# Kernel optimization log

Measured on AMD Instinct MI355X. Metric: run time of the kernel, lower is better.

The kernel has to match this reference:

```python
import jax, jax.numpy as jnp
import numpy as np

EPS = 1e-6
C = 0.05            # curvature
TEMPERATURE = 0.1
ALPHA_D = 0.5       # current_epoch = 0 -> alpha stays at init value


def setup_inputs() -> dict:
    key = jax.random.key(0)
    k1, k2 = jax.random.split(key)
    B, D = 1024, 128
    # scale so norms stay well inside the Poincare ball (radius 1/sqrt(c) ~ 4.47)
    z_hyp = jax.random.normal(k1, (B, D), dtype=jnp.float32) * 0.05
    z_hyp_prime = jax.random.normal(k2, (B, D), dtype=jnp.float32) * 0.05
    return {"z_hyp": z_hyp, "z_hyp_prime": z_hyp_prime}


def _pairwise_hyp_distance(zx, zy, c):
    """d(x_i, y_j) = 2/sqrt(c) * atanh(sqrt(c) * ||mobius_add(-x_i, y_j)||) for all pairs."""
    x = -zx[:, None, :]          # [B, 1, D]  (neg_x in the original)
    y = zy[None, :, :]           # [1, B, D]
    x2 = jnp.sum(x * x, axis=-1, keepdims=True)   # [B, 1, 1]
    y2 = jnp.sum(y * y, axis=-1, keepdims=True)   # [1, B, 1]
    xy = jnp.sum(x * y, axis=-1, keepdims=True)   # [B, B, 1]
    num = (1.0 + 2.0 * c * xy + c * y2) * x + (1.0 - c * x2) * y   # [B, B, D]
    den = jnp.maximum(1.0 + 2.0 * c * xy + (c ** 2) * x2 * y2, EPS)
    m = num / den
    mnorm = jnp.sqrt(jnp.sum(m * m, axis=-1))      # [B, B]
    sqrt_c = np.sqrt(c).astype(np.float32)
    return (2.0 / sqrt_c) * jnp.arctanh(jnp.minimum(sqrt_c * mnorm, 1.0 - EPS))


def reference(z_hyp, z_hyp_prime):
    B = z_hyp.shape[0]
    distances = _pairwise_hyp_distance(z_hyp, z_hyp_prime, C)      # [B, B]
    distance_sim = -distances / TEMPERATURE

    # angle-based similarity (cosine, F.normalize with eps=1e-12)
    zn = z_hyp / jnp.maximum(jnp.linalg.norm(z_hyp, axis=1, keepdims=True), 1e-12)
    zpn = z_hyp_prime / jnp.maximum(jnp.linalg.norm(z_hyp_prime, axis=1, keepdims=True), 1e-12)
    angle_sim = (zn @ zpn.T) / TEMPERATURE

    combined_sim = ALPHA_D * distance_sim + (1.0 - ALPHA_D) * angle_sim

    # unsupervised InfoNCE-style loss: positives on the diagonal, diagonal
    # excluded from the denominator (faithful to the original code)
    pos_sim = jnp.diagonal(combined_sim)                           # [B]
    exp_sim = jnp.exp(combined_sim) * (1.0 - jnp.eye(B, dtype=combined_sim.dtype))
    denom = jnp.sum(exp_sim, axis=1)                               # [B]
    loss = jnp.mean(-pos_sim + jnp.log(denom))
    return loss
```

## Files before the change

kernel.cpp:

```cpp
#include <hip/hip_runtime.h>
#include <math.h>

#define B_ROWS 1024
#define D_DIM 128
#define DCHUNKS 32

__device__ __forceinline__ float dot4(float4 a, float4 b) {
  return fmaf(a.x, b.x, fmaf(a.y, b.y, fmaf(a.z, b.z, a.w * b.w)));
}

#define K_C 0.05f
#define K_SQRT_C 0.22360679774997896f
#define K_INV_SQRT_C 4.47213595499958f
#define K_EPS 1e-6f
#define K_HALF_INV_T 5.0f

__global__ __launch_bounds__(1024) void hypcd_pair(const float* __restrict__ za,
                                                   const float* __restrict__ zb,
                                                   float* __restrict__ out) {
  __shared__ float s_a[4 * D_DIM];
  __shared__ float s_x2[4];
  __shared__ float s_pos[4];
  __shared__ float s_esum[4];
  __shared__ float s_rl[4];

  const int tid = threadIdx.x;
  const int i0 = blockIdx.x * 4;

  if (tid < (4 * D_DIM / 4)) {
    reinterpret_cast<float4*>(s_a)[tid] =
        reinterpret_cast<const float4*>(za + (size_t)i0 * D_DIM)[tid];
  }
  if (tid < 4) s_esum[tid] = 0.0f;
  __syncthreads();

  const int wave = tid >> 6;
  const int lane = tid & 63;

  if (wave < 4) {
    float v0 = s_a[wave * D_DIM + lane];
    float v1 = s_a[wave * D_DIM + lane + 64];
    float s = fmaf(v0, v0, v1 * v1);
#pragma unroll
    for (int m = 32; m >= 1; m >>= 1) s += __shfl_xor(s, m);
    if (lane == 0) s_x2[wave] = s;
  }
  __syncthreads();

  float x2v[4], rnxv[4];
#pragma unroll
  for (int i = 0; i < 4; ++i) {
    x2v[i] = s_x2[i];
    rnxv[i] = __frsqrt_rn(fmaxf(x2v[i], 1e-24f));
  }

  const int dg = lane & 7;
  const int jg = lane >> 3;
  const int b0 = dg & 1, b1 = (dg >> 1) & 1, b2 = (dg >> 2) & 1;
  const int pbase = (b0 << 3) | (b1 << 2) | (b2 << 1);
  const int isel = pbase >> 2;
  const int jj0 = pbase & 3;

  const float x2i = b0 ? (b1 ? x2v[3] : x2v[2]) : (b1 ? x2v[1] : x2v[0]);
  const float rnxi = b0 ? (b1 ? rnxv[3] : rnxv[2]) : (b1 ? rnxv[1] : rnxv[0]);

  float my_esum = 0.0f;
  const float4* bp = reinterpret_cast<const float4*>(zb);

#pragma unroll
  for (int pass = 0; pass < 2; ++pass) {
    const int jb = pass * 512 + wave * 32 + jg * 4;

    float v[16];
    float y2p[4];
#pragma unroll
    for (int k = 0; k < 16; ++k) v[k] = 0.0f;
#pragma unroll
    for (int k = 0; k < 4; ++k) y2p[k] = 0.0f;

#pragma unroll
    for (int dstep = 0; dstep < 4; ++dstep) {
      const int dc = dstep * 8 + dg;
      float4 bv0 = bp[(jb + 0) * DCHUNKS + dc];
      float4 bv1 = bp[(jb + 1) * DCHUNKS + dc];
      float4 bv2 = bp[(jb + 2) * DCHUNKS + dc];
      float4 bv3 = bp[(jb + 3) * DCHUNKS + dc];
#pragma unroll
      for (int i = 0; i < 4; ++i) {
        float4 av = reinterpret_cast<const float4*>(s_a + i * D_DIM)[dc];
        v[i * 4 + 0] += dot4(av, bv0);
        v[i * 4 + 1] += dot4(av, bv1);
        v[i * 4 + 2] += dot4(av, bv2);
        v[i * 4 + 3] += dot4(av, bv3);
      }
      y2p[0] += dot4(bv0, bv0);
      y2p[1] += dot4(bv1, bv1);
      y2p[2] += dot4(bv2, bv2);
      y2p[3] += dot4(bv3, bv3);
    }

    {
      float q0keep = b2 ? y2p[2] : y2p[0];
      float q0send = b2 ? y2p[0] : y2p[2];
      float q1keep = b2 ? y2p[3] : y2p[1];
      float q1send = b2 ? y2p[1] : y2p[3];
      y2p[0] = q0keep + __shfl_xor(q0send, 4);
      y2p[1] = q1keep + __shfl_xor(q1send, 4);
#pragma unroll
      for (int m = 1; m <= 2; m <<= 1) {
        y2p[0] += __shfl_xor(y2p[0], m);
        y2p[1] += __shfl_xor(y2p[1], m);
      }
    }
    const float y2s0 = y2p[0];
    const float y2s1 = y2p[1];

    float w8[8];
#pragma unroll
    for (int k = 0; k < 8; ++k) {
      float mine = b0 ? v[8 + k] : v[k];
      float theirs = b0 ? v[k] : v[8 + k];
      w8[k] = mine + __shfl_xor(theirs, 1);
    }
    float w4[4];
#pragma unroll
    for (int k = 0; k < 4; ++k) {
      float mine = b1 ? w8[4 + k] : w8[k];
      float theirs = b1 ? w8[k] : w8[4 + k];
      w4[k] = mine + __shfl_xor(theirs, 2);
    }
    float w2[2];
#pragma unroll
    for (int k = 0; k < 2; ++k) {
      float mine = b2 ? w4[2 + k] : w4[k];
      float theirs = b2 ? w4[k] : w4[2 + k];
      w2[k] = mine + __shfl_xor(theirs, 4);
    }

#pragma unroll
    for (int pp = 0; pp < 2; ++pp) {
      const float g = (pp == 0) ? w2[0] : w2[1];
      const float y2 = (pp == 0) ? y2s0 : y2s1;
      const int gj = jb + jj0 + pp;
      const int gi = i0 + isel;

      const float xy = -g;
      const float Am = fmaf(2.0f * K_C, xy, fmaf(K_C, y2, 1.0f));
      const float Bm = fmaf(-K_C, x2i, 1.0f);
      const float den =
          fmaxf(fmaf(2.0f * K_C, xy, fmaf(K_C * K_C * x2i, y2, 1.0f)), K_EPS);
      const float num2 =
          fmaf(Am * Am, x2i, fmaf(2.0f * Am * Bm, xy, Bm * Bm * y2));
      const float mnorm = __fdividef(sqrtf(fmaxf(num2, 0.0f)), den);
      const float t = fminf(K_SQRT_C * mnorm, 1.0f - K_EPS);
      const float dist = K_INV_SQRT_C * __logf(__fdividef(1.0f + t, 1.0f - t));
      const float rny = __frsqrt_rn(fmaxf(y2, 1e-24f));
      const float comb = K_HALF_INV_T * fmaf(g * rnxi, rny, -dist);

      if (gi == gj) {
        s_pos[isel] = comb;
      } else {
        my_esum += __expf(comb);
      }
    }
  }

#pragma unroll
  for (int m = 8; m <= 32; m <<= 1) my_esum += __shfl_xor(my_esum, m);
  if (jg == 0) atomicAdd(&s_esum[isel], my_esum);
  __syncthreads();

  if (tid < 4) {
    s_rl[tid] = __logf(s_esum[tid]) - s_pos[tid];
  }
  __syncthreads();
  if (tid == 0) {
    atomicAdd(out, (s_rl[0] + s_rl[1] + s_rl[2] + s_rl[3]) * (1.0f / 1024.0f));
  }
}

extern "C" void kernel_launch(void* const* d_in, const int* in_sizes, int n_in,
                              void* d_out, int out_size, void* d_ws, size_t ws_size,
                              hipStream_t stream) {
  const float* za = (const float*)d_in[0];
  const float* zb = (const float*)d_in[1];
  (void)hipMemsetAsync(d_out, 0, sizeof(float), stream);
  hypcd_pair<<<B_ROWS / 4, 1024, 0, stream>>>(za, zb, (float*)d_out);
}
```

Baseline: 68.17 us.

## Replace memset and atomic accumulation with cooperative grid sync reduction

Drops the separate memset launch by writing per-block partial losses to the workspace. A cooperative grid sync follows, and block 0 then reduces the partials deterministically. It also folds the division by den into the log ratio, saving a divide per pair. The grid-wide barrier costs every block and needs all 256 blocks of 1024 threads to be resident at once.

```diff
diff --git a/kernel.cpp b/kernel.cpp
--- a/kernel.cpp
+++ b/kernel.cpp
@@ -1,9 +1,13 @@
 #include <hip/hip_runtime.h>
+#include <hip/hip_cooperative_groups.h>
 #include <math.h>
+
+namespace cg = cooperative_groups;
 
 #define B_ROWS 1024
 #define D_DIM 128
 #define DCHUNKS 32
+#define NBLOCKS (B_ROWS / 4)
 
 __device__ __forceinline__ float dot4(float4 a, float4 b) {
   return fmaf(a.x, b.x, fmaf(a.y, b.y, fmaf(a.z, b.z, a.w * b.w)));
@@ -17,6 +21,7 @@
 
 __global__ __launch_bounds__(1024) void hypcd_pair(const float* __restrict__ za,
                                                    const float* __restrict__ zb,
+                                                   float* __restrict__ partials,
                                                    float* __restrict__ out) {
   __shared__ float s_a[4 * D_DIM];
   __shared__ float s_x2[4];
@@ -151,9 +156,9 @@
           fmaxf(fmaf(2.0f * K_C, xy, fmaf(K_C * K_C * x2i, y2, 1.0f)), K_EPS);
       const float num2 =
           fmaf(Am * Am, x2i, fmaf(2.0f * Am * Bm, xy, Bm * Bm * y2));
-      const float mnorm = __fdividef(sqrtf(fmaxf(num2, 0.0f)), den);
-      const float t = fminf(K_SQRT_C * mnorm, 1.0f - K_EPS);
-      const float dist = K_INV_SQRT_C * __logf(__fdividef(1.0f + t, 1.0f - t));
+      const float u =
+          fminf(K_SQRT_C * sqrtf(fmaxf(num2, 0.0f)), (1.0f - K_EPS) * den);
+      const float dist = K_INV_SQRT_C * __logf(__fdividef(den + u, den - u));
       const float rny = __frsqrt_rn(fmaxf(y2, 1e-24f));
       const float comb = K_HALF_INV_T * fmaf(g * rnxi, rny, -dist);
 
@@ -175,7 +180,25 @@
   }
   __syncthreads();
   if (tid == 0) {
-    atomicAdd(out, (s_rl[0] + s_rl[1] + s_rl[2] + s_rl[3]) * (1.0f / 1024.0f));
+    __hip_atomic_store(&partials[blockIdx.x],
+                       s_rl[0] + s_rl[1] + s_rl[2] + s_rl[3], __ATOMIC_RELEASE,
+                       __HIP_MEMORY_SCOPE_AGENT);
+  }
+
+  cg::this_grid().sync();
+
+  if (blockIdx.x == 0 && tid < 64) {
+    float v = __hip_atomic_load(&partials[tid], __ATOMIC_ACQUIRE,
+                                __HIP_MEMORY_SCOPE_AGENT) +
+              __hip_atomic_load(&partials[tid + 64], __ATOMIC_ACQUIRE,
+                                __HIP_MEMORY_SCOPE_AGENT) +
+              __hip_atomic_load(&partials[tid + 128], __ATOMIC_ACQUIRE,
+                                __HIP_MEMORY_SCOPE_AGENT) +
+              __hip_atomic_load(&partials[tid + 192], __ATOMIC_ACQUIRE,
+                                __HIP_MEMORY_SCOPE_AGENT);
+#pragma unroll
+    for (int m = 32; m >= 1; m >>= 1) v += __shfl_xor(v, m);
+    if (tid == 0) out[0] = v * (1.0f / 1024.0f);
   }
 }
 
@@ -184,6 +207,10 @@
                               hipStream_t stream) {
   const float* za = (const float*)d_in[0];
   const float* zb = (const float*)d_in[1];
-  (void)hipMemsetAsync(d_out, 0, sizeof(float), stream);
-  hypcd_pair<<<B_ROWS / 4, 1024, 0, stream>>>(za, zb, (float*)d_out);
+  float* partials = (float*)d_ws;
+  float* outp = (float*)d_out;
+
+  void* args[] = {(void*)&za, (void*)&zb, (void*)&partials, (void*)&outp};
+  (void)hipLaunchCooperativeKernel((const void*)hypcd_pair, dim3(NBLOCKS),
+                                   dim3(1024), args, 0, stream);
 }
```

New measurement: 103.2 us. 51.3% more time.
